# Optimization experiments

Measured on AMD Instinct MI355X. Metric: run time of the kernel, lower is better.

## Reference

```python
import jax, jax.numpy as jnp
import numpy as np

B, N0 = 16384, 2048
NUM_CLASSES, NUM_CLUSTERS, NDIM = 12, 24, 4
W_SCALE = 0.02  # keep logits in a sane range for softmax


def setup_inputs() -> dict:
    key = jax.random.key(0)
    ks = jax.random.split(key, 7)
    return {
        "x": jax.random.normal(ks[0], (B, N0), dtype=jnp.float32),
        "W_fc": jax.random.normal(ks[1], (N0, NUM_CLASSES), dtype=jnp.float32) * W_SCALE,
        "b_fc": jax.random.normal(ks[2], (NUM_CLASSES,), dtype=jnp.float32) * W_SCALE,
        "W_bin": jax.random.normal(ks[3], (NUM_CLASSES, N0, NUM_CLUSTERS), dtype=jnp.float32) * W_SCALE,
        "b_bin": jax.random.normal(ks[4], (NUM_CLASSES, NUM_CLUSTERS), dtype=jnp.float32) * W_SCALE,
        "W_res": jax.random.normal(ks[5], (NUM_CLASSES, N0, NDIM), dtype=jnp.float32) * W_SCALE,
        "b_res": jax.random.normal(ks[6], (NUM_CLASSES, NDIM), dtype=jnp.float32) * W_SCALE,
    }


def reference(x, W_fc, b_fc, W_bin, b_bin, W_res, b_res):
    # x: [B, N0] pre-extracted features (feature_model output)
    bsz = x.shape[0]
    C = W_bin.shape[0]

    # category head
    y0 = x @ W_fc + b_fc                                   # [B, C]
    Pc = jax.nn.softmax(y0, axis=1)                        # [B, C]

    # grouped per-class bin linears as one batched GEMM -> [B, K, C]
    y1 = jnp.einsum('bd,cdk->bkc', x, W_bin) + b_bin.T[None]
    Pl = jax.nn.softmax(y1, axis=1)                        # softmax over clusters
    Plc = Pl * Pc[:, None, :]                              # [B, K, C]

    # joint argmax over (cluster, class); torch flatten of [B,K,C] -> ic = ind % C
    ind = jnp.argmax(Plc.reshape(bsz, -1), axis=1)
    ic = ind % C                                           # selected class per row

    # direct gather replaces one-hot scatter + bmm
    y1_sel = jnp.take_along_axis(y1, ic[:, None, None], axis=2)[..., 0]   # [B, K]

    # grouped per-class residual linears -> [B, ndim, C], then gather
    y2 = jnp.einsum('bd,cdn->bnc', x, W_res) + b_res.T[None]
    y2_sel = jnp.take_along_axis(y2, ic[:, None, None], axis=2)[..., 0]   # [B, ndim]

    return (y0, y1_sel, y2_sel, Plc)
```

## Files before the change

### kernel.cpp

```cpp
#include <hip/hip_runtime.h>
#include <math.h>

#define BROWS 16384
#define N0    2048
#define NCLS  12
#define NCLU  24
#define NDIM  4
#define NCOL  348
#define NPAD  384
#define NTILE 24

#define OUT0_OFF 0
#define OUT1_OFF (BROWS * NCLS)
#define OUT2_OFF (OUT1_OFF + BROWS * NCLU)
#define OUT3_OFF (OUT2_OFF + BROWS * NDIM)

typedef __attribute__((ext_vector_type(8))) short bf16x8;
typedef __attribute__((ext_vector_type(4))) float f32x4;
typedef unsigned short ushort_t;

__device__ __forceinline__ unsigned short f2bf(float f) {
    unsigned u = __float_as_uint(f);
    u += 0x7fffu + ((u >> 16) & 1u);
    return (unsigned short)(u >> 16);
}
__device__ __forceinline__ float bf2f(unsigned short h) {
    return __uint_as_float(((unsigned)h) << 16);
}
__device__ __forceinline__ void cvt8(float4 a, float4 b, bf16x8& h, bf16x8& l) {
    float f[8] = {a.x, a.y, a.z, a.w, b.x, b.y, b.z, b.w};
    #pragma unroll
    for (int i = 0; i < 8; ++i) {
        unsigned short hi = f2bf(f[i]);
        h[i] = (short)hi;
        l[i] = (short)f2bf(f[i] - bf2f(hi));
    }
}

__device__ __forceinline__ void cvt8pk(float4 a, float4 b, bf16x8& h, bf16x8& l) {
    unsigned h0, h1, h2, h3;
    asm("v_cvt_pk_bf16_f32 %0, %1, %2" : "=v"(h0) : "v"(a.x), "v"(a.y));
    asm("v_cvt_pk_bf16_f32 %0, %1, %2" : "=v"(h1) : "v"(a.z), "v"(a.w));
    asm("v_cvt_pk_bf16_f32 %0, %1, %2" : "=v"(h2) : "v"(b.x), "v"(b.y));
    asm("v_cvt_pk_bf16_f32 %0, %1, %2" : "=v"(h3) : "v"(b.z), "v"(b.w));
    float r0 = a.x - __uint_as_float(h0 << 16);
    float r1 = a.y - __uint_as_float(h0 & 0xffff0000u);
    float r2 = a.z - __uint_as_float(h1 << 16);
    float r3 = a.w - __uint_as_float(h1 & 0xffff0000u);
    float r4 = b.x - __uint_as_float(h2 << 16);
    float r5 = b.y - __uint_as_float(h2 & 0xffff0000u);
    float r6 = b.z - __uint_as_float(h3 << 16);
    float r7 = b.w - __uint_as_float(h3 & 0xffff0000u);
    unsigned l0, l1, l2, l3;
    asm("v_cvt_pk_bf16_f32 %0, %1, %2" : "=v"(l0) : "v"(r0), "v"(r1));
    asm("v_cvt_pk_bf16_f32 %0, %1, %2" : "=v"(l1) : "v"(r2), "v"(r3));
    asm("v_cvt_pk_bf16_f32 %0, %1, %2" : "=v"(l2) : "v"(r4), "v"(r5));
    asm("v_cvt_pk_bf16_f32 %0, %1, %2" : "=v"(l3) : "v"(r6), "v"(r7));
    union Pack { unsigned u[4]; bf16x8 v; };
    Pack H; H.u[0] = h0; H.u[1] = h1; H.u[2] = h2; H.u[3] = h3;
    Pack L; L.u[0] = l0; L.u[1] = l1; L.u[2] = l2; L.u[3] = l3;
    h = H.v;
    l = L.v;
}

__device__ __forceinline__ void load_lds16(const void* g, void* l) {
    __builtin_amdgcn_global_load_lds((const __attribute__((address_space(1))) void*)g,
                                     (__attribute__((address_space(3))) void*)l, 16, 0, 0);
}

__device__ __forceinline__ float fused_w(const float* __restrict__ W_fc,
                                         const float* __restrict__ W_bin,
                                         const float* __restrict__ W_res,
                                         int col, int d) {
    float w = 0.0f;
    if (col < NCLS) {
        w = W_fc[d * NCLS + col];
    } else if (col < 12 + NCLU * NCLS) {
        int jj = col - 12;
        int k = jj / NCLS, c = jj - k * NCLS;
        w = W_bin[((size_t)c * N0 + d) * NCLU + k];
    } else if (col < NCOL) {
        int jj = col - 300;
        int n = jj / NCLS, c = jj - n * NCLS;
        w = W_res[((size_t)c * N0 + d) * NDIM + n];
    }
    return w;
}

__global__ void jcp_repack3(const float* __restrict__ W_fc, const float* __restrict__ b_fc,
                            const float* __restrict__ W_bin, const float* __restrict__ b_bin,
                            const float* __restrict__ W_res, const float* __restrict__ b_res,
                            ushort_t* __restrict__ Bph, ushort_t* __restrict__ Bpl,
                            float* __restrict__ bias) {
    int t = blockIdx.x * 256 + threadIdx.x;
    if (t >= NTILE * 64 * 64) return;
    const int lane = t & 63;
    const int kb   = (t >> 6) & 63;
    const int J    = t >> 12;
    const int col  = J * 16 + (lane & 15);
    const int k0   = kb * 32 + (lane >> 4) * 8;

    bf16x8 h, l;
    #pragma unroll
    for (int i = 0; i < 8; ++i) {
        float w = fused_w(W_fc, W_bin, W_res, col, k0 + i);
        unsigned short hi = f2bf(w);
        h[i] = (short)hi;
        l[i] = (short)f2bf(w - bf2f(hi));
    }
    *(bf16x8*)(Bph + (size_t)t * 8) = h;
    *(bf16x8*)(Bpl + (size_t)t * 8) = l;

    if (t < NPAD) {
        int jb = t;
        float bv = 0.0f;
        if (jb < NCLS) {
            bv = b_fc[jb];
        } else if (jb < 12 + NCLU * NCLS) {
            int jj = jb - 12;
            int k = jj / NCLS, c = jj - k * NCLS;
            bv = b_bin[c * NCLU + k];
        } else if (jb < NCOL) {
            int jj = jb - 300;
            int n = jj / NCLS, c = jj - n * NCLS;
            bv = b_res[c * NDIM + n];
        }
        bias[jb] = bv;
    }
}

__global__ __launch_bounds__(256, 2) void jcp_gemm9(const float* __restrict__ x,
                                                    const ushort_t* __restrict__ Bph,
                                                    const ushort_t* __restrict__ Bpl,
                                                    const float* __restrict__ bias,
                                                    float* __restrict__ Y) {
    __shared__ float    Lx[2 * 4096];
    __shared__ ushort_t Lb[2 * 6144];

    const int tid  = threadIdx.x;
    const int wid  = tid >> 6;
    const int lane = tid & 63;
    const int quad = lane >> 4;
    const int l16  = lane & 15;
    const int rg   = wid & 1;
    const int cg   = wid >> 1;

    const int g   = blockIdx.x;
    const int xcd = g & 7;
    const int jj  = g >> 3;
    const int by  = xcd * 16 + (jj >> 2);
    const int bx  = jj & 3;
    const int rbase = by * 128;
    const int jbase = bx * 96;

    const int r0 = tid >> 3;
    const int c0 = tid & 7;
    const int o0 = c0 ^ (r0 & 7);
    const float* gx = x + (size_t)(rbase + r0) * N0 + o0 * 4;

    const ushort_t* gb[3];
    int bdst[3];
    #pragma unroll
    for (int m = 0; m < 3; ++m) {
        const int c  = m * 4 + wid;
        const int J  = bx * 6 + (c >> 1);
        const ushort_t* bp = (c & 1) ? Bpl : Bph;
        gb[m]   = bp + (size_t)J * 32768 + lane * 8;
        bdst[m] = c * 512 + lane * 8;
    }

    const int s  = l16 & 7;
    const int o1 = ((2 * quad) ^ s) * 4;
    const int o2 = o1 ^ 4;

    f32x4 acc[4][3];
    #pragma unroll
    for (int rt = 0; rt < 4; ++rt)
        #pragma unroll
        for (int j = 0; j < 3; ++j)
            acc[rt][j] = f32x4{0.f, 0.f, 0.f, 0.f};

    #pragma unroll
    for (int n = 0; n < 4; ++n) load_lds16(gx + n * 65536, &Lx[n * 1024 + tid * 4]);
    #pragma unroll
    for (int m = 0; m < 3; ++m) load_lds16(gb[m], &Lb[bdst[m]]);
    #pragma unroll
    for (int n = 0; n < 4; ++n) load_lds16(gx + n * 65536 + 32, &Lx[4096 + n * 1024 + tid * 4]);
    #pragma unroll
    for (int m = 0; m < 3; ++m) load_lds16(gb[m] + 512, &Lb[6144 + bdst[m]]);

    int p = 0;
    for (int it = 0; it < 63; ++it) {
        asm volatile("s_waitcnt vmcnt(7)" ::: "memory");
        asm volatile("s_barrier" ::: "memory");

        const float*    lx = &Lx[p * 4096];
        const ushort_t* lb = &Lb[p * 6144];

        float4 fa[4], fb[4];
        #pragma unroll
        for (int rt = 0; rt < 4; ++rt) {
            const int ro = (rg * 64 + rt * 16 + l16) * 32;
            fa[rt] = *(const float4*)&lx[ro + o1];
            fb[rt] = *(const float4*)&lx[ro + o2];
        }
        bf16x8 bh[3], bl[3];
        #pragma unroll
        for (int j = 0; j < 3; ++j) {
            const int ch = (cg * 3 + j) * 2;
            bh[j] = *(const bf16x8*)(lb + ch * 512 + lane * 8);
            bl[j] = *(const bf16x8*)(lb + ch * 512 + 512 + lane * 8);
        }
        asm volatile("s_waitcnt lgkmcnt(0)" ::: "memory");
        asm volatile("s_barrier" ::: "memory");

        if (it < 62) {
            #pragma unroll
            for (int n = 0; n < 4; ++n)
                load_lds16(gx + n * 65536 + (it + 2) * 32,
                           &Lx[p * 4096 + n * 1024 + tid * 4]);
            #pragma unroll
            for (int m = 0; m < 3; ++m)
                load_lds16(gb[m] + (it + 2) * 512, &Lb[p * 6144 + bdst[m]]);
        }

        bf16x8 Ah[4], Al[4];
        #pragma unroll
        for (int rt = 0; rt < 4; ++rt) cvt8pk(fa[rt], fb[rt], Ah[rt], Al[rt]);

        __builtin_amdgcn_s_setprio(1);
        #pragma unroll
        for (int j = 0; j < 3; ++j)
            #pragma unroll
            for (int rt = 0; rt < 4; ++rt) {
                acc[rt][j] = __builtin_amdgcn_mfma_f32_16x16x32_bf16(Ah[rt], bh[j], acc[rt][j], 0, 0, 0);
                acc[rt][j] = __builtin_amdgcn_mfma_f32_16x16x32_bf16(Al[rt], bh[j], acc[rt][j], 0, 0, 0);
                acc[rt][j] = __builtin_amdgcn_mfma_f32_16x16x32_bf16(Ah[rt], bl[j], acc[rt][j], 0, 0, 0);
            }
        __builtin_amdgcn_s_setprio(0);
        p ^= 1;
    }

    {
        asm volatile("s_waitcnt vmcnt(0)" ::: "memory");
        asm volatile("s_barrier" ::: "memory");
        const float*    lx = &Lx[p * 4096];
        const ushort_t* lb = &Lb[p * 6144];
        bf16x8 Ah[4], Al[4];
        #pragma unroll
        for (int rt = 0; rt < 4; ++rt) {
            const int ro = (rg * 64 + rt * 16 + l16) * 32;
            float4 fa = *(const float4*)&lx[ro + o1];
            float4 fb = *(const float4*)&lx[ro + o2];
            cvt8pk(fa, fb, Ah[rt], Al[rt]);
        }
        bf16x8 bh[3], bl[3];
        #pragma unroll
        for (int j = 0; j < 3; ++j) {
            const int ch = (cg * 3 + j) * 2;
            bh[j] = *(const bf16x8*)(lb + ch * 512 + lane * 8);
            bl[j] = *(const bf16x8*)(lb + ch * 512 + 512 + lane * 8);
        }
        #pragma unroll
        for (int j = 0; j < 3; ++j)
            #pragma unroll
            for (int rt = 0; rt < 4; ++rt) {
                acc[rt][j] = __builtin_amdgcn_mfma_f32_16x16x32_bf16(Ah[rt], bh[j], acc[rt][j], 0, 0, 0);
                acc[rt][j] = __builtin_amdgcn_mfma_f32_16x16x32_bf16(Al[rt], bh[j], acc[rt][j], 0, 0, 0);
                acc[rt][j] = __builtin_amdgcn_mfma_f32_16x16x32_bf16(Ah[rt], bl[j], acc[rt][j], 0, 0, 0);
            }
    }

    #pragma unroll
    for (int j = 0; j < 3; ++j) {
        const int col = jbase + cg * 48 + 16 * j + l16;
        const float bj = bias[col];
        #pragma unroll
        for (int rt = 0; rt < 4; ++rt) {
            float* yp = Y + (size_t)(rbase + rg * 64 + rt * 16 + quad * 4) * NPAD + col;
            yp[0 * NPAD] = acc[rt][j][0] + bj;
            yp[1 * NPAD] = acc[rt][j][1] + bj;
            yp[2 * NPAD] = acc[rt][j][2] + bj;
            yp[3 * NPAD] = acc[rt][j][3] + bj;
        }
    }
}

#define LROW 388

__global__ __launch_bounds__(256) void jcp_head4(const float* __restrict__ Y,
                                                 float* __restrict__ out) {
    __shared__ float Ly[16 * LROW];
    const int tid = threadIdx.x;
    const int r0  = blockIdx.x * 16;

    #pragma unroll
    for (int jj = 0; jj < 6; ++jj) {
        int f = tid + jj * 256;
        int row = f / 96, c4 = f - row * 96;
        float4 v = *(const float4*)(Y + (size_t)(r0 + row) * NPAD + c4 * 4);
        *(float4*)&Ly[row * LROW + c4 * 4] = v;
    }
    __syncthreads();

    const int grp = tid >> 4;
    const int c   = tid & 15;
    const bool on = (c < NCLS);
    const int r   = r0 + grp;
    const float* y = &Ly[grp * LROW];

    float y0c = on ? y[c] : -INFINITY;
    float m0 = y0c;
    #pragma unroll
    for (int m = 8; m >= 1; m >>= 1) m0 = fmaxf(m0, __shfl_xor(m0, m, 16));
    float e0 = on ? expf(y0c - m0) : 0.0f;
    float s0 = e0;
    #pragma unroll
    for (int m = 8; m >= 1; m >>= 1) s0 += __shfl_xor(s0, m, 16);
    const float Pc = e0 / s0;

    float v[NCLU];
    float mc = -INFINITY;
    #pragma unroll
    for (int k = 0; k < NCLU; ++k) {
        v[k] = y[12 + k * NCLS + c];
        mc = fmaxf(mc, v[k]);
    }
    float ev[NCLU];
    float sc = 0.0f;
    #pragma unroll
    for (int k = 0; k < NCLU; ++k) { ev[k] = expf(v[k] - mc); sc += ev[k]; }
    const float rs = Pc / sc;

    float y2c[NDIM];
    #pragma unroll
    for (int n = 0; n < NDIM; ++n) y2c[n] = y[300 + n * NCLS + c];

    float best = -INFINITY;
    int bk = 0;
    float* lrow = &Ly[grp * LROW];
    #pragma unroll
    for (int k = 0; k < NCLU; ++k) {
        const float p = ev[k] * rs;
        if (on) lrow[k * NCLS + c] = p;
        if (p > best) { best = p; bk = k; }
    }
    int flat = bk * NCLS + c;
    if (!on) { best = -INFINITY; flat = 1 << 30; }

    #pragma unroll
    for (int m = 8; m >= 1; m >>= 1) {
        const float op = __shfl_xor(best, m, 16);
        const int   of = __shfl_xor(flat, m, 16);
        if (op > best || (op == best && of < flat)) { best = op; flat = of; }
    }
    const int ic = flat % NCLS;

    if (on) out[OUT0_OFF + (size_t)r * NCLS + c] = y0c;
    if (c == ic) {
        float* o1 = out + OUT1_OFF + (size_t)r * NCLU;
        #pragma unroll
        for (int k = 0; k < NCLU; ++k) o1[k] = v[k];
        float* o2 = out + OUT2_OFF + (size_t)r * NDIM;
        #pragma unroll
        for (int n = 0; n < NDIM; ++n) o2[n] = y2c[n];
    }

    __syncthreads();
    #pragma unroll
    for (int jj = 0; jj < 5; ++jj) {
        int f = tid + jj * 256;
        if (f < 1152) {
            int row = f / 72, c4 = f - row * 72;
            *(float4*)(out + OUT3_OFF + (size_t)(r0 + row) * (NCLU * NCLS) + c4 * 4) =
                *(float4*)&Ly[row * LROW + c4 * 4];
        }
    }
}

extern "C" void kernel_launch(void* const* d_in, const int* in_sizes, int n_in,
                              void* d_out, int out_size, void* d_ws, size_t ws_size,
                              hipStream_t stream) {
    const float* x     = (const float*)d_in[0];
    const float* W_fc  = (const float*)d_in[1];
    const float* b_fc  = (const float*)d_in[2];
    const float* W_bin = (const float*)d_in[3];
    const float* b_bin = (const float*)d_in[4];
    const float* W_res = (const float*)d_in[5];
    const float* b_res = (const float*)d_in[6];
    float* out = (float*)d_out;

    ushort_t* Bph  = (ushort_t*)d_ws;
    ushort_t* Bpl  = Bph + NTILE * 64 * 64 * 8;
    float*    bias = (float*)(Bpl + NTILE * 64 * 64 * 8);
    float*    Yb   = bias + NPAD;

    jcp_repack3<<<384, 256, 0, stream>>>(W_fc, b_fc, W_bin, b_bin, W_res, b_res,
                                         Bph, Bpl, bias);
    jcp_gemm9<<<512, 256, 0, stream>>>(x, Bph, Bpl, bias, Yb);
    jcp_head4<<<BROWS / 16, 256, 0, stream>>>(Yb, out);
}
```

Baseline: 268.1 us.

## Software-pipeline GEMM loop so fragment loads and conversion precede next MFMA block

Restructures the main K loop of the split-bf16 GEMM into a prologue, steady state and epilogue. Fragments for the next step are read from LDS and converted to hi/lo bf16 at the end of each iteration, and the MFMA block runs right after the next global-to-LDS loads are issued. The aim is to take the LDS reads and conversion off the critical path between barriers and overlap the global loads with MFMA work. In exchange, the fragments stay live across iterations, which raises register pressure, and the buffer-index logic becomes more involved.

```diff
diff --git a/kernel.cpp b/kernel.cpp
--- a/kernel.cpp
+++ b/kernel.cpp
@@ -26,15 +26,6 @@
 }
 __device__ __forceinline__ float bf2f(unsigned short h) {
     return __uint_as_float(((unsigned)h) << 16);
-}
-__device__ __forceinline__ void cvt8(float4 a, float4 b, bf16x8& h, bf16x8& l) {
-    float f[8] = {a.x, a.y, a.z, a.w, b.x, b.y, b.z, b.w};
-    #pragma unroll
-    for (int i = 0; i < 8; ++i) {
-        unsigned short hi = f2bf(f[i]);
-        h[i] = (short)hi;
-        l[i] = (short)f2bf(f[i] - bf2f(hi));
-    }
 }
 
 __device__ __forceinline__ void cvt8pk(float4 a, float4 b, bf16x8& h, bf16x8& l) {
@@ -129,11 +120,11 @@
     }
 }
 
-__global__ __launch_bounds__(256, 2) void jcp_gemm9(const float* __restrict__ x,
-                                                    const ushort_t* __restrict__ Bph,
-                                                    const ushort_t* __restrict__ Bpl,
-                                                    const float* __restrict__ bias,
-                                                    float* __restrict__ Y) {
+__global__ __launch_bounds__(256, 2) void jcp_gemm11(const float* __restrict__ x,
+                                                     const ushort_t* __restrict__ Bph,
+                                                     const ushort_t* __restrict__ Bpl,
+                                                     const float* __restrict__ bias,
+                                                     float* __restrict__ Y) {
     __shared__ float    Lx[2 * 4096];
     __shared__ ushort_t Lb[2 * 6144];
 
@@ -180,6 +171,8 @@
         for (int j = 0; j < 3; ++j)
             acc[rt][j] = f32x4{0.f, 0.f, 0.f, 0.f};
 
+    bf16x8 Ah[4], Al[4], bh[3], bl[3];
+
     #pragma unroll
     for (int n = 0; n < 4; ++n) load_lds16(gx + n * 65536, &Lx[n * 1024 + tid * 4]);
     #pragma unroll
@@ -188,15 +181,11 @@
     for (int n = 0; n < 4; ++n) load_lds16(gx + n * 65536 + 32, &Lx[4096 + n * 1024 + tid * 4]);
     #pragma unroll
     for (int m = 0; m < 3; ++m) load_lds16(gb[m] + 512, &Lb[6144 + bdst[m]]);
-
-    int p = 0;
-    for (int it = 0; it < 63; ++it) {
-        asm volatile("s_waitcnt vmcnt(7)" ::: "memory");
-        asm volatile("s_barrier" ::: "memory");
-
-        const float*    lx = &Lx[p * 4096];
-        const ushort_t* lb = &Lb[p * 6144];
-
+    asm volatile("s_waitcnt vmcnt(7)" ::: "memory");
+    asm volatile("s_barrier" ::: "memory");
+    {
+        const float*    lx = &Lx[0];
+        const ushort_t* lb = &Lb[0];
         float4 fa[4], fb[4];
         #pragma unroll
         for (int rt = 0; rt < 4; ++rt) {
@@ -204,7 +193,6 @@
             fa[rt] = *(const float4*)&lx[ro + o1];
             fb[rt] = *(const float4*)&lx[ro + o2];
         }
-        bf16x8 bh[3], bl[3];
         #pragma unroll
         for (int j = 0; j < 3; ++j) {
             const int ch = (cg * 3 + j) * 2;
@@ -212,21 +200,21 @@
             bl[j] = *(const bf16x8*)(lb + ch * 512 + 512 + lane * 8);
         }
         asm volatile("s_waitcnt lgkmcnt(0)" ::: "memory");
+        #pragma unroll
+        for (int rt = 0; rt < 4; ++rt) cvt8pk(fa[rt], fb[rt], Ah[rt], Al[rt]);
         asm volatile("s_barrier" ::: "memory");
-
-        if (it < 62) {
-            #pragma unroll
-            for (int n = 0; n < 4; ++n)
-                load_lds16(gx + n * 65536 + (it + 2) * 32,
-                           &Lx[p * 4096 + n * 1024 + tid * 4]);
-            #pragma unroll
-            for (int m = 0; m < 3; ++m)
-                load_lds16(gb[m] + (it + 2) * 512, &Lb[p * 6144 + bdst[m]]);
-        }
-
-        bf16x8 Ah[4], Al[4];
-        #pragma unroll
-        for (int rt = 0; rt < 4; ++rt) cvt8pk(fa[rt], fb[rt], Ah[rt], Al[rt]);
+    }
+
+    int p = 0;
+    for (int it = 0; it < 62; ++it) {
+        #pragma unroll
+        for (int n = 0; n < 4; ++n)
+            load_lds16(gx + n * 65536 + (it + 2) * 32,
+                       &Lx[p * 4096 + n * 1024 + tid * 4]);
+        #pragma unroll
+        for (int m = 0; m < 3; ++m)
+            load_lds16(gb[m] + (it + 2) * 512, &Lb[p * 6144 + bdst[m]]);
+        __builtin_amdgcn_sched_barrier(0);
 
         __builtin_amdgcn_s_setprio(1);
         #pragma unroll
@@ -238,29 +226,63 @@
                 acc[rt][j] = __builtin_amdgcn_mfma_f32_16x16x32_bf16(Ah[rt], bl[j], acc[rt][j], 0, 0, 0);
             }
         __builtin_amdgcn_s_setprio(0);
-        p ^= 1;
-    }
-
-    {
-        asm volatile("s_waitcnt vmcnt(0)" ::: "memory");
+
+        asm volatile("s_waitcnt vmcnt(7)" ::: "memory");
         asm volatile("s_barrier" ::: "memory");
-        const float*    lx = &Lx[p * 4096];
-        const ushort_t* lb = &Lb[p * 6144];
-        bf16x8 Ah[4], Al[4];
+
+        const float*    lx = &Lx[(p ^ 1) * 4096];
+        const ushort_t* lb = &Lb[(p ^ 1) * 6144];
+        float4 fa[4], fb[4];
         #pragma unroll
         for (int rt = 0; rt < 4; ++rt) {
             const int ro = (rg * 64 + rt * 16 + l16) * 32;
-            float4 fa = *(const float4*)&lx[ro + o1];
-            float4 fb = *(const float4*)&lx[ro + o2];
-            cvt8pk(fa, fb, Ah[rt], Al[rt]);
-        }
-        bf16x8 bh[3], bl[3];
+            fa[rt] = *(const float4*)&lx[ro + o1];
+            fb[rt] = *(const float4*)&lx[ro + o2];
+        }
         #pragma unroll
         for (int j = 0; j < 3; ++j) {
             const int ch = (cg * 3 + j) * 2;
             bh[j] = *(const bf16x8*)(lb + ch * 512 + lane * 8);
             bl[j] = *(const bf16x8*)(lb + ch * 512 + 512 + lane * 8);
         }
+        asm volatile("s_waitcnt lgkmcnt(0)" ::: "memory");
+        #pragma unroll
+        for (int rt = 0; rt < 4; ++rt) cvt8pk(fa[rt], fb[rt], Ah[rt], Al[rt]);
+        asm volatile("s_barrier" ::: "memory");
+        p ^= 1;
+    }
+
+    {
+        __builtin_amdgcn_s_setprio(1);
+        #pragma unroll
+        for (int j = 0; j < 3; ++j)
+            #pragma unroll
+            for (int rt = 0; rt < 4; ++rt) {
+                acc[rt][j] = __builtin_amdgcn_mfma_f32_16x16x32_bf16(Ah[rt], bh[j], acc[rt][j], 0, 0, 0);
+                acc[rt][j] = __builtin_amdgcn_mfma_f32_16x16x32_bf16(Al[rt], bh[j], acc[rt][j], 0, 0, 0);
+                acc[rt][j] = __builtin_amdgcn_mfma_f32_16x16x32_bf16(Ah[rt], bl[j], acc[rt][j], 0, 0, 0);
+            }
+        __builtin_amdgcn_s_setprio(0);
+        asm volatile("s_waitcnt vmcnt(0)" ::: "memory");
+        asm volatile("s_barrier" ::: "memory");
+        const float*    lx = &Lx[(p ^ 1) * 4096];
+        const ushort_t* lb = &Lb[(p ^ 1) * 6144];
+        float4 fa[4], fb[4];
+        #pragma unroll
+        for (int rt = 0; rt < 4; ++rt) {
+            const int ro = (rg * 64 + rt * 16 + l16) * 32;
+            fa[rt] = *(const float4*)&lx[ro + o1];
+            fb[rt] = *(const float4*)&lx[ro + o2];
+        }
+        #pragma unroll
+        for (int j = 0; j < 3; ++j) {
+            const int ch = (cg * 3 + j) * 2;
+            bh[j] = *(const bf16x8*)(lb + ch * 512 + lane * 8);
+            bl[j] = *(const bf16x8*)(lb + ch * 512 + 512 + lane * 8);
+        }
+        asm volatile("s_waitcnt lgkmcnt(0)" ::: "memory");
+        #pragma unroll
+        for (int rt = 0; rt < 4; ++rt) cvt8pk(fa[rt], fb[rt], Ah[rt], Al[rt]);
         #pragma unroll
         for (int j = 0; j < 3; ++j)
             #pragma unroll
@@ -397,6 +419,6 @@
 
     jcp_repack3<<<384, 256, 0, stream>>>(W_fc, b_fc, W_bin, b_bin, W_res, b_res,
                                          Bph, Bpl, bias);
-    jcp_gemm9<<<512, 256, 0, stream>>>(x, Bph, Bpl, bias, Yb);
+    jcp_gemm11<<<512, 256, 0, stream>>>(x, Bph, Bpl, bias, Yb);
     jcp_head4<<<BROWS / 16, 256, 0, stream>>>(Yb, out);
 }
```

New measurement: 274.5 us. 1.02x slower.

## Load B fragments directly to registers and software-pipeline GEMM with register double buffering

Applied to the files above, without the earlier changes.

Packed weight fragments are no longer staged through shared memory. Each wave now loads its own bh/bl fragments straight from global memory into double-buffered registers one step ahead. The main loop is unrolled by two, so the MFMAs for the current k-step overlap with loading and converting the next x tile, using scheduling barriers and explicit vmcnt waits. This cuts LDS traffic and one barrier phase per iteration, but it raises register pressure and makes correctness depend on hand-tuned wait counts.

```diff
diff --git a/kernel.cpp b/kernel.cpp
--- a/kernel.cpp
+++ b/kernel.cpp
@@ -26,15 +26,6 @@
 }
 __device__ __forceinline__ float bf2f(unsigned short h) {
     return __uint_as_float(((unsigned)h) << 16);
-}
-__device__ __forceinline__ void cvt8(float4 a, float4 b, bf16x8& h, bf16x8& l) {
-    float f[8] = {a.x, a.y, a.z, a.w, b.x, b.y, b.z, b.w};
-    #pragma unroll
-    for (int i = 0; i < 8; ++i) {
-        unsigned short hi = f2bf(f[i]);
-        h[i] = (short)hi;
-        l[i] = (short)f2bf(f[i] - bf2f(hi));
-    }
 }
 
 __device__ __forceinline__ void cvt8pk(float4 a, float4 b, bf16x8& h, bf16x8& l) {
@@ -129,13 +120,61 @@
     }
 }
 
-__global__ __launch_bounds__(256, 2) void jcp_gemm9(const float* __restrict__ x,
-                                                    const ushort_t* __restrict__ Bph,
-                                                    const ushort_t* __restrict__ Bpl,
-                                                    const float* __restrict__ bias,
-                                                    float* __restrict__ Y) {
-    __shared__ float    Lx[2 * 4096];
-    __shared__ ushort_t Lb[2 * 6144];
+#define GBODY(CUR, NXT, PBUF, RBUF, IT)                                        \
+    {                                                                          \
+        _Pragma("unroll")                                                      \
+        for (int j = 0; j < 3; ++j) {                                          \
+            bh[NXT][j] = *(const bf16x8*)(pBh + Jt3[j] + ((IT) + 1) * 512);    \
+            bl[NXT][j] = *(const bf16x8*)(pBl + Jt3[j] + ((IT) + 1) * 512);    \
+        }                                                                      \
+        __builtin_amdgcn_sched_barrier(0);                                     \
+        _Pragma("unroll")                                                      \
+        for (int n = 0; n < 4; ++n)                                            \
+            load_lds16(gx + n * 65536 + ((IT) + 2) * 32,                       \
+                       &Lx[(PBUF) * 4096 + n * 1024 + tid * 4]);               \
+        __builtin_amdgcn_sched_barrier(0);                                     \
+        __builtin_amdgcn_s_setprio(1);                                         \
+        _Pragma("unroll")                                                      \
+        for (int j = 0; j < 3; ++j) {                                          \
+            _Pragma("unroll")                                                  \
+            for (int rt = 0; rt < 4; ++rt) {                                   \
+                acc[rt][j] = __builtin_amdgcn_mfma_f32_16x16x32_bf16(          \
+                    Ah[CUR][rt], bh[CUR][j], acc[rt][j], 0, 0, 0);             \
+                acc[rt][j] = __builtin_amdgcn_mfma_f32_16x16x32_bf16(          \
+                    Al[CUR][rt], bh[CUR][j], acc[rt][j], 0, 0, 0);             \
+                acc[rt][j] = __builtin_amdgcn_mfma_f32_16x16x32_bf16(          \
+                    Ah[CUR][rt], bl[CUR][j], acc[rt][j], 0, 0, 0);             \
+            }                                                                  \
+        }                                                                      \
+        __builtin_amdgcn_s_setprio(0);                                         \
+        asm volatile("s_waitcnt vmcnt(10)" ::: "memory");                      \
+        asm volatile("s_barrier" ::: "memory");                                \
+        __builtin_amdgcn_sched_barrier(0);                                     \
+        {                                                                      \
+            const float* lx = &Lx[(RBUF) * 4096];                              \
+            _Pragma("unroll")                                                  \
+            for (int rt = 0; rt < 4; ++rt) {                                   \
+                const int ro = (rg * 64 + rt * 16 + l16) * 32;                 \
+                fa4[rt] = *(const float4*)&lx[ro + o1];                        \
+                fb4[rt] = *(const float4*)&lx[ro + o2];                        \
+            }                                                                  \
+            asm volatile("s_waitcnt lgkmcnt(0)" ::: "memory");                 \
+            __builtin_amdgcn_sched_barrier(0);                                 \
+            _Pragma("unroll")                                                  \
+            for (int rt = 0; rt < 4; ++rt)                                     \
+                cvt8pk(fa4[rt], fb4[rt], Ah[NXT][rt], Al[NXT][rt]);            \
+        }                                                                      \
+        asm volatile("s_waitcnt vmcnt(4)" ::: "memory");                       \
+        __builtin_amdgcn_sched_barrier(0);                                     \
+        asm volatile("s_barrier" ::: "memory");                                \
+    }
+
+__global__ __launch_bounds__(256, 2) void jcp_gemm12(const float* __restrict__ x,
+                                                     const ushort_t* __restrict__ Bph,
+                                                     const ushort_t* __restrict__ Bpl,
+                                                     const float* __restrict__ bias,
+                                                     float* __restrict__ Y) {
+    __shared__ float Lx[2 * 4096];
 
     const int tid  = threadIdx.x;
     const int wid  = tid >> 6;
@@ -158,16 +197,11 @@
     const int o0 = c0 ^ (r0 & 7);
     const float* gx = x + (size_t)(rbase + r0) * N0 + o0 * 4;
 
-    const ushort_t* gb[3];
-    int bdst[3];
-    #pragma unroll
-    for (int m = 0; m < 3; ++m) {
-        const int c  = m * 4 + wid;
-        const int J  = bx * 6 + (c >> 1);
-        const ushort_t* bp = (c & 1) ? Bpl : Bph;
-        gb[m]   = bp + (size_t)J * 32768 + lane * 8;
-        bdst[m] = c * 512 + lane * 8;
-    }
+    const ushort_t* pBh = Bph + (size_t)lane * 8;
+    const ushort_t* pBl = Bpl + (size_t)lane * 8;
+    int Jt3[3];
+    #pragma unroll
+    for (int j = 0; j < 3; ++j) Jt3[j] = (bx * 6 + cg * 3 + j) * 32768;
 
     const int s  = l16 & 7;
     const int o1 = ((2 * quad) ^ s) * 4;
@@ -180,94 +214,86 @@
         for (int j = 0; j < 3; ++j)
             acc[rt][j] = f32x4{0.f, 0.f, 0.f, 0.f};
 
+    bf16x8 Ah[2][4], Al[2][4], bh[2][3], bl[2][3];
+    float4 fa4[4], fb4[4];
+
     #pragma unroll
     for (int n = 0; n < 4; ++n) load_lds16(gx + n * 65536, &Lx[n * 1024 + tid * 4]);
-    #pragma unroll
-    for (int m = 0; m < 3; ++m) load_lds16(gb[m], &Lb[bdst[m]]);
+    __builtin_amdgcn_sched_barrier(0);
+    #pragma unroll
+    for (int j = 0; j < 3; ++j) {
+        bh[0][j] = *(const bf16x8*)(pBh + Jt3[j]);
+        bl[0][j] = *(const bf16x8*)(pBl + Jt3[j]);
+    }
+    __builtin_amdgcn_sched_barrier(0);
     #pragma unroll
     for (int n = 0; n < 4; ++n) load_lds16(gx + n * 65536 + 32, &Lx[4096 + n * 1024 + tid * 4]);
-    #pragma unroll
-    for (int m = 0; m < 3; ++m) load_lds16(gb[m] + 512, &Lb[6144 + bdst[m]]);
-
-    int p = 0;
-    for (int it = 0; it < 63; ++it) {
-        asm volatile("s_waitcnt vmcnt(7)" ::: "memory");
-        asm volatile("s_barrier" ::: "memory");
-
-        const float*    lx = &Lx[p * 4096];
-        const ushort_t* lb = &Lb[p * 6144];
-
-        float4 fa[4], fb[4];
+    __builtin_amdgcn_sched_barrier(0);
+    asm volatile("s_waitcnt vmcnt(10)" ::: "memory");
+    asm volatile("s_barrier" ::: "memory");
+    __builtin_amdgcn_sched_barrier(0);
+    {
+        const float* lx = &Lx[0];
         #pragma unroll
         for (int rt = 0; rt < 4; ++rt) {
             const int ro = (rg * 64 + rt * 16 + l16) * 32;
-            fa[rt] = *(const float4*)&lx[ro + o1];
-            fb[rt] = *(const float4*)&lx[ro + o2];
-        }
-        bf16x8 bh[3], bl[3];
+            fa4[rt] = *(const float4*)&lx[ro + o1];
+            fb4[rt] = *(const float4*)&lx[ro + o2];
+        }
+        asm volatile("s_waitcnt lgkmcnt(0)" ::: "memory");
+        __builtin_amdgcn_sched_barrier(0);
+        #pragma unroll
+        for (int rt = 0; rt < 4; ++rt) cvt8pk(fa4[rt], fb4[rt], Ah[0][rt], Al[0][rt]);
+    }
+    asm volatile("s_waitcnt vmcnt(4)" ::: "memory");
+    __builtin_amdgcn_sched_barrier(0);
+    asm volatile("s_barrier" ::: "memory");
+
+    for (int it = 0; it < 62; it += 2) {
+        GBODY(0, 1, 0, 1, it);
+        GBODY(1, 0, 1, 0, it + 1);
+    }
+
+    {
         #pragma unroll
         for (int j = 0; j < 3; ++j) {
-            const int ch = (cg * 3 + j) * 2;
-            bh[j] = *(const bf16x8*)(lb + ch * 512 + lane * 8);
-            bl[j] = *(const bf16x8*)(lb + ch * 512 + 512 + lane * 8);
-        }
-        asm volatile("s_waitcnt lgkmcnt(0)" ::: "memory");
-        asm volatile("s_barrier" ::: "memory");
-
-        if (it < 62) {
-            #pragma unroll
-            for (int n = 0; n < 4; ++n)
-                load_lds16(gx + n * 65536 + (it + 2) * 32,
-                           &Lx[p * 4096 + n * 1024 + tid * 4]);
-            #pragma unroll
-            for (int m = 0; m < 3; ++m)
-                load_lds16(gb[m] + (it + 2) * 512, &Lb[p * 6144 + bdst[m]]);
-        }
-
-        bf16x8 Ah[4], Al[4];
-        #pragma unroll
-        for (int rt = 0; rt < 4; ++rt) cvt8pk(fa[rt], fb[rt], Ah[rt], Al[rt]);
-
+            bh[1][j] = *(const bf16x8*)(pBh + Jt3[j] + 63 * 512);
+            bl[1][j] = *(const bf16x8*)(pBl + Jt3[j] + 63 * 512);
+        }
+        __builtin_amdgcn_sched_barrier(0);
         __builtin_amdgcn_s_setprio(1);
         #pragma unroll
         for (int j = 0; j < 3; ++j)
             #pragma unroll
             for (int rt = 0; rt < 4; ++rt) {
-                acc[rt][j] = __builtin_amdgcn_mfma_f32_16x16x32_bf16(Ah[rt], bh[j], acc[rt][j], 0, 0, 0);
-                acc[rt][j] = __builtin_amdgcn_mfma_f32_16x16x32_bf16(Al[rt], bh[j], acc[rt][j], 0, 0, 0);
-                acc[rt][j] = __builtin_amdgcn_mfma_f32_16x16x32_bf16(Ah[rt], bl[j], acc[rt][j], 0, 0, 0);
+                acc[rt][j] = __builtin_amdgcn_mfma_f32_16x16x32_bf16(Ah[0][rt], bh[0][j], acc[rt][j], 0, 0, 0);
+                acc[rt][j] = __builtin_amdgcn_mfma_f32_16x16x32_bf16(Al[0][rt], bh[0][j], acc[rt][j], 0, 0, 0);
+                acc[rt][j] = __builtin_amdgcn_mfma_f32_16x16x32_bf16(Ah[0][rt], bl[0][j], acc[rt][j], 0, 0, 0);
             }
         __builtin_amdgcn_s_setprio(0);
-        p ^= 1;
-    }
-
-    {
-        asm volatile("s_waitcnt vmcnt(0)" ::: "memory");
+        asm volatile("s_waitcnt vmcnt(6)" ::: "memory");
         asm volatile("s_barrier" ::: "memory");
-        const float*    lx = &Lx[p * 4096];
-        const ushort_t* lb = &Lb[p * 6144];
-        bf16x8 Ah[4], Al[4];
+        __builtin_amdgcn_sched_barrier(0);
+        const float* lx = &Lx[4096];
         #pragma unroll
         for (int rt = 0; rt < 4; ++rt) {
             const int ro = (rg * 64 + rt * 16 + l16) * 32;
-            float4 fa = *(const float4*)&lx[ro + o1];
-            float4 fb = *(const float4*)&lx[ro + o2];
-            cvt8pk(fa, fb, Ah[rt], Al[rt]);
-        }
-        bf16x8 bh[3], bl[3];
-        #pragma unroll
-        for (int j = 0; j < 3; ++j) {
-            const int ch = (cg * 3 + j) * 2;
-            bh[j] = *(const bf16x8*)(lb + ch * 512 + lane * 8);
-            bl[j] = *(const bf16x8*)(lb + ch * 512 + 512 + lane * 8);
-        }
+            fa4[rt] = *(const float4*)&lx[ro + o1];
+            fb4[rt] = *(const float4*)&lx[ro + o2];
+        }
+        asm volatile("s_waitcnt lgkmcnt(0)" ::: "memory");
+        __builtin_amdgcn_sched_barrier(0);
+        #pragma unroll
+        for (int rt = 0; rt < 4; ++rt) cvt8pk(fa4[rt], fb4[rt], Ah[1][rt], Al[1][rt]);
+        asm volatile("s_waitcnt vmcnt(0)" ::: "memory");
+        __builtin_amdgcn_sched_barrier(0);
         #pragma unroll
         for (int j = 0; j < 3; ++j)
             #pragma unroll
             for (int rt = 0; rt < 4; ++rt) {
-                acc[rt][j] = __builtin_amdgcn_mfma_f32_16x16x32_bf16(Ah[rt], bh[j], acc[rt][j], 0, 0, 0);
-                acc[rt][j] = __builtin_amdgcn_mfma_f32_16x16x32_bf16(Al[rt], bh[j], acc[rt][j], 0, 0, 0);
-                acc[rt][j] = __builtin_amdgcn_mfma_f32_16x16x32_bf16(Ah[rt], bl[j], acc[rt][j], 0, 0, 0);
+                acc[rt][j] = __builtin_amdgcn_mfma_f32_16x16x32_bf16(Ah[1][rt], bh[1][j], acc[rt][j], 0, 0, 0);
+                acc[rt][j] = __builtin_amdgcn_mfma_f32_16x16x32_bf16(Al[1][rt], bh[1][j], acc[rt][j], 0, 0, 0);
+                acc[rt][j] = __builtin_amdgcn_mfma_f32_16x16x32_bf16(Ah[1][rt], bl[1][j], acc[rt][j], 0, 0, 0);
             }
     }
 
@@ -358,12 +384,12 @@
 
     if (on) out[OUT0_OFF + (size_t)r * NCLS + c] = y0c;
     if (c == ic) {
-        float* o1 = out + OUT1_OFF + (size_t)r * NCLU;
-        #pragma unroll
-        for (int k = 0; k < NCLU; ++k) o1[k] = v[k];
-        float* o2 = out + OUT2_OFF + (size_t)r * NDIM;
-        #pragma unroll
-        for (int n = 0; n < NDIM; ++n) o2[n] = y2c[n];
+        float* o1v = out + OUT1_OFF + (size_t)r * NCLU;
+        #pragma unroll
+        for (int k = 0; k < NCLU; ++k) o1v[k] = v[k];
+        float* o2v = out + OUT2_OFF + (size_t)r * NDIM;
+        #pragma unroll
+        for (int n = 0; n < NDIM; ++n) o2v[n] = y2c[n];
     }
 
     __syncthreads();
@@ -397,6 +423,6 @@
 
     jcp_repack3<<<384, 256, 0, stream>>>(W_fc, b_fc, W_bin, b_bin, W_res, b_res,
                                          Bph, Bpl, bias);
-    jcp_gemm9<<<512, 256, 0, stream>>>(x, Bph, Bpl, bias, Yb);
+    jcp_gemm12<<<512, 256, 0, stream>>>(x, Bph, Bpl, bias, Yb);
     jcp_head4<<<BROWS / 16, 256, 0, stream>>>(Yb, out);
 }
```

Result: slower. 274.0 us (+2.2%).
